# Kernel optimization log

Measured on AMD Instinct MI355X. Metric: run time of the kernel, lower is better.

Reference implementation:

```python
import jax, jax.numpy as jnp
import numpy as np

BATCH, N_MACS_PREV, CMS_PREV, NEUR_PREV = 256, 512, 8, 16
FILTER_LEN = 256
NUM_CMS, NUM_NEURONS = 32, 32
NUM_INPUTS = FILTER_LEN * CMS_PREV * NEUR_PREV  # 32768


def setup_inputs() -> dict:
    key = jax.random.key(0)
    k1, k2, k3 = jax.random.split(key, 3)
    x = jax.random.uniform(k1, (BATCH, N_MACS_PREV, CMS_PREV, NEUR_PREV), dtype=jnp.float32)
    input_filter = jax.random.randint(k2, (FILTER_LEN,), 0, N_MACS_PREV)
    # binary {0,1} weights, matching torch.randint(0, 2, ..., dtype=float32)
    weights = jax.random.randint(k3, (NUM_CMS, NUM_INPUTS, NUM_NEURONS), 0, 2).astype(jnp.float32)
    return {"x": x, "input_filter": input_filter, "weights": weights}


def reference(x, input_filter, weights):
    B = x.shape[0]
    # gather receptive field MACs and flatten: (B, num_inputs)
    xg = jnp.take(x, input_filter, axis=1).reshape(B, -1)
    # sum-normalize, nan_to_num handles all-zero rows (0/0 -> 0)
    xn = jnp.nan_to_num(xg / jnp.sum(xg, axis=-1, keepdims=True))
    # batched matmul: (B,I) x (C,I,N) -> (B,C,N)  (torch does (C,B,N) then permutes)
    acts = jnp.einsum('bi,cin->bcn', xn, weights)
    # familiarity-based softmax temperature
    familiarities = jnp.max(acts, axis=-1)          # (B, C)
    avg_fam = jnp.mean(familiarities)               # scalar
    softmax_temp = 1.0 / (avg_fam + 1e-4) - 1.0
    logits = acts / softmax_temp
    # categorical sample per (batch, cm); fixed key for determinism
    samples = jax.random.categorical(jax.random.key(42), logits, axis=-1)  # (B, C)
    # scatter one-hot write-out, int output as in torch
    out = jax.nn.one_hot(samples, NUM_NEURONS, dtype=jnp.int32)  # (B, C, N)
    return out
```

## Files before the change

### kernel.cpp

```cpp
#include <hip/hip_runtime.h>
#include <stdint.h>

#define BATCH 256
#define NMAC  512
#define ROWF  128
#define I_    32768
#define C_    32
#define N_    32
#define XROW  (NMAC * ROWF)
#define NCH   64

typedef float  f32x4  __attribute__((ext_vector_type(4)));
typedef __bf16 bf16x8 __attribute__((ext_vector_type(8)));

__device__ __forceinline__ uint32_t f2bf_rne(float f) {
    uint32_t u = __builtin_bit_cast(uint32_t, f);
    return (u + 0x7FFFu + ((u >> 16) & 1u)) >> 16;
}

__global__ __launch_bounds__(256) void k_sum(const float* __restrict__ x,
                                             const int* __restrict__ filt,
                                             float* __restrict__ S) {
    const int b = blockIdx.x;
    const int t = threadIdx.x;
    const float* xb = x + (size_t)b * XROW;
    float s = 0.f;
    for (int it = 0; it < 32; ++it) {
        int idx4 = it * 256 + t;
        int f = idx4 >> 5;
        int j4 = idx4 & 31;
        float4 v = *(const float4*)(xb + (size_t)filt[f] * ROWF + j4 * 4);
        s += v.x + v.y + v.z + v.w;
    }
    for (int o = 32; o > 0; o >>= 1) s += __shfl_down(s, o, 64);
    __shared__ float red[4];
    if ((t & 63) == 0) red[t >> 6] = s;
    __syncthreads();
    if (t == 0) S[b] = red[0] + red[1] + red[2] + red[3];
}

__global__ __launch_bounds__(256, 2) void k_gemm5(const float* __restrict__ x,
                                                  const int* __restrict__ filt,
                                                  const float* __restrict__ w,
                                                  float* __restrict__ part) {
    __shared__ __align__(16) unsigned short afr[32 * 512];
    __shared__ __align__(16) unsigned short wfr[8 * 512];
    __shared__ uint32_t wbits[4 * 512];

    const int t  = threadIdx.x;
    const int l  = t & 63;
    const int wv = t >> 6;
    const int chunk = blockIdx.x & 63;
    const int c0 = (blockIdx.x >> 6) * 4;

    f32x4 acc[4][8];
#pragma unroll
    for (int bt = 0; bt < 4; ++bt)
#pragma unroll
        for (int ct = 0; ct < 8; ++ct) acc[bt][ct] = f32x4{0.f, 0.f, 0.f, 0.f};

#pragma unroll
    for (int j = 0; j < 8; ++j) {
        int r  = j * 256 + t;
        int c  = r & 3;
        int io = r >> 2;
        const float4* wp = (const float4*)(w +
            ((size_t)(c0 + c) * I_ + chunk * 512 + io) * N_);
        uint32_t m = 0;
#pragma unroll
        for (int q = 0; q < 8; ++q) {
            float4 v = wp[q];
            m |= (v.x != 0.f ? 1u : 0u) << (q * 4 + 0);
            m |= (v.y != 0.f ? 1u : 0u) << (q * 4 + 1);
            m |= (v.z != 0.f ? 1u : 0u) << (q * 4 + 2);
            m |= (v.w != 0.f ? 1u : 0u) << (q * 4 + 3);
        }
        wbits[c * 512 + io] = m;
    }
    __syncthreads();

    const int ar     = t >> 3;
    const int ai     = t & 7;
    const int a_quad = ai >> 1;
    const int a_j    = (ai & 1) * 4;
    const int wn = t & 31;
    const int wc = t >> 5;

    for (int st = 0; st < 16; ++st) {
        const int ifull = chunk * 512 + st * 32;
        const int fidx  = filt[ifull >> 7];
        const int ioff  = ifull & 127;
        const float* xs = x + (size_t)fidx * ROWF + ioff;

#pragma unroll
        for (int q = 0; q < 8; ++q) {
            int sl = wc + 8 * q;
            int c  = sl >> 4;
            int il = (sl & 15) * 2;
            uint2 mm = *(const uint2*)&wbits[c * 512 + st * 32 + il];
            uint32_t pk = (((mm.x >> wn) & 1u) ? 0x00003F80u : 0u)
                        | (((mm.y >> wn) & 1u) ? 0x3F800000u : 0u);
            int lane = (il >> 3) * 16 + (wn & 15);
            int ct   = c * 2 + (wn >> 4);
            *(uint32_t*)&wfr[ct * 512 + lane * 8 + (il & 7)] = pk;
        }

#pragma unroll
        for (int rr = 0; rr < 8; ++rr) {
            int row = rr * 32 + ar;
            float4 v = *(const float4*)(xs + (size_t)row * XROW + ai * 4);
            uint32_t u0 = __builtin_bit_cast(uint32_t, v.x);
            uint32_t u1 = __builtin_bit_cast(uint32_t, v.y);
            uint32_t u2 = __builtin_bit_cast(uint32_t, v.z);
            uint32_t u3 = __builtin_bit_cast(uint32_t, v.w);
            float l0 = v.x - __builtin_bit_cast(float, u0 & 0xFFFF0000u);
            float l1 = v.y - __builtin_bit_cast(float, u1 & 0xFFFF0000u);
            float l2 = v.z - __builtin_bit_cast(float, u2 & 0xFFFF0000u);
            float l3 = v.w - __builtin_bit_cast(float, u3 & 0xFFFF0000u);
            uint2 hp, lp;
            hp.x = (u0 >> 16) | (u1 & 0xFFFF0000u);
            hp.y = (u2 >> 16) | (u3 & 0xFFFF0000u);
            lp.x = f2bf_rne(l0) | (f2bf_rne(l1) << 16);
            lp.y = f2bf_rne(l2) | (f2bf_rne(l3) << 16);
            int rt   = row >> 4;
            int lane = a_quad * 16 + (row & 15);
            int base = (rt * 2) * 512 + lane * 8 + a_j;
            *(uint2*)&afr[base]       = hp;
            *(uint2*)&afr[base + 512] = lp;
        }
        __syncthreads();

        bf16x8 av[4][2];
#pragma unroll
        for (int bt = 0; bt < 4; ++bt)
#pragma unroll
            for (int p = 0; p < 2; ++p)
                av[bt][p] = *(const bf16x8*)&afr[((wv * 4 + bt) * 2 + p) * 512 + l * 8];
        bf16x8 bv[8];
#pragma unroll
        for (int ct = 0; ct < 8; ++ct)
            bv[ct] = *(const bf16x8*)&wfr[ct * 512 + l * 8];
#pragma unroll
        for (int bt = 0; bt < 4; ++bt)
#pragma unroll
            for (int ct = 0; ct < 8; ++ct) {
                acc[bt][ct] = __builtin_amdgcn_mfma_f32_16x16x32_bf16(av[bt][0], bv[ct], acc[bt][ct], 0, 0, 0);
                acc[bt][ct] = __builtin_amdgcn_mfma_f32_16x16x32_bf16(av[bt][1], bv[ct], acc[bt][ct], 0, 0, 0);
            }
        __syncthreads();
    }

    const int quad = l >> 4, n15 = l & 15;
    float* dst = part + (size_t)chunk * (BATCH * C_ * N_);
#pragma unroll
    for (int bt = 0; bt < 4; ++bt) {
#pragma unroll
        for (int ct = 0; ct < 8; ++ct) {
            int c = c0 + (ct >> 1);
            int n = (ct & 1) * 16 + n15;
#pragma unroll
            for (int r = 0; r < 4; ++r) {
                int b = (wv * 4 + bt) * 16 + quad * 4 + r;
                dst[((size_t)b * C_ + c) * N_ + n] = acc[bt][ct][r];
            }
        }
    }
}

__global__ __launch_bounds__(256, 2) void k_gemm_fb(const float* __restrict__ x,
                                                    const int* __restrict__ filt,
                                                    const float* __restrict__ w,
                                                    float* __restrict__ raw) {
    __shared__ __align__(16) unsigned short afr[32 * 512];
    __shared__ __align__(16) unsigned short wfr[8 * 512];

    const int t  = threadIdx.x;
    const int l  = t & 63;
    const int wv = t >> 6;
    const int chunk = blockIdx.x & 63;
    const int c0 = (blockIdx.x >> 6) * 4;

    f32x4 acc[4][8];
#pragma unroll
    for (int bt = 0; bt < 4; ++bt)
#pragma unroll
        for (int ct = 0; ct < 8; ++ct) acc[bt][ct] = f32x4{0.f, 0.f, 0.f, 0.f};

    const int ar     = t >> 3;
    const int ai     = t & 7;
    const int a_quad = ai >> 1;
    const int a_j    = (ai & 1) * 4;
    const int wn = t & 31;
    const int wc = t >> 5;

    for (int st = 0; st < 16; ++st) {
        const int ifull = chunk * 512 + st * 32;
        const int fidx  = filt[ifull >> 7];
        const int ioff  = ifull & 127;
        const float* xs = x + (size_t)fidx * ROWF + ioff;

#pragma unroll
        for (int rr = 0; rr < 8; ++rr) {
            int row = rr * 32 + ar;
            float4 v = *(const float4*)(xs + (size_t)row * XROW + ai * 4);
            uint32_t u0 = __builtin_bit_cast(uint32_t, v.x);
            uint32_t u1 = __builtin_bit_cast(uint32_t, v.y);
            uint32_t u2 = __builtin_bit_cast(uint32_t, v.z);
            uint32_t u3 = __builtin_bit_cast(uint32_t, v.w);
            float l0 = v.x - __builtin_bit_cast(float, u0 & 0xFFFF0000u);
            float l1 = v.y - __builtin_bit_cast(float, u1 & 0xFFFF0000u);
            float l2 = v.z - __builtin_bit_cast(float, u2 & 0xFFFF0000u);
            float l3 = v.w - __builtin_bit_cast(float, u3 & 0xFFFF0000u);
            uint2 hp, lp;
            hp.x = (u0 >> 16) | (u1 & 0xFFFF0000u);
            hp.y = (u2 >> 16) | (u3 & 0xFFFF0000u);
            lp.x = f2bf_rne(l0) | (f2bf_rne(l1) << 16);
            lp.y = f2bf_rne(l2) | (f2bf_rne(l3) << 16);
            int rt   = row >> 4;
            int lane = a_quad * 16 + (row & 15);
            int base = (rt * 2) * 512 + lane * 8 + a_j;
            *(uint2*)&afr[base]       = hp;
            *(uint2*)&afr[base + 512] = lp;
        }
#pragma unroll
        for (int q = 0; q < 8; ++q) {
            int sl  = wc + 8 * q;
            int c   = sl >> 4;
            int il  = (sl & 15) * 2;
            const float* wp = w + ((size_t)(c0 + c) * I_ + ifull + il) * N_ + wn;
            uint32_t u0 = __builtin_bit_cast(uint32_t, wp[0]);
            uint32_t u1 = __builtin_bit_cast(uint32_t, wp[N_]);
            uint32_t pk = (u0 >> 16) | (u1 & 0xFFFF0000u);
            int lane = (il >> 3) * 16 + (wn & 15);
            int ct   = c * 2 + (wn >> 4);
            *(uint32_t*)&wfr[ct * 512 + lane * 8 + (il & 7)] = pk;
        }
        __syncthreads();

        bf16x8 av[4][2];
#pragma unroll
        for (int bt = 0; bt < 4; ++bt)
#pragma unroll
            for (int p = 0; p < 2; ++p)
                av[bt][p] = *(const bf16x8*)&afr[((wv * 4 + bt) * 2 + p) * 512 + l * 8];
        bf16x8 bv[8];
#pragma unroll
        for (int ct = 0; ct < 8; ++ct)
            bv[ct] = *(const bf16x8*)&wfr[ct * 512 + l * 8];
#pragma unroll
        for (int bt = 0; bt < 4; ++bt)
#pragma unroll
            for (int ct = 0; ct < 8; ++ct) {
                acc[bt][ct] = __builtin_amdgcn_mfma_f32_16x16x32_bf16(av[bt][0], bv[ct], acc[bt][ct], 0, 0, 0);
                acc[bt][ct] = __builtin_amdgcn_mfma_f32_16x16x32_bf16(av[bt][1], bv[ct], acc[bt][ct], 0, 0, 0);
            }
        __syncthreads();
    }

    const int quad = l >> 4, n15 = l & 15;
#pragma unroll
    for (int bt = 0; bt < 4; ++bt)
#pragma unroll
        for (int ct = 0; ct < 8; ++ct) {
            int c = c0 + (ct >> 1);
            int n = (ct & 1) * 16 + n15;
#pragma unroll
            for (int r = 0; r < 4; ++r) {
                int b = (wv * 4 + bt) * 16 + quad * 4 + r;
                atomicAdd(&raw[((size_t)b * C_ + c) * N_ + n], acc[bt][ct][r]);
            }
        }
}

__global__ __launch_bounds__(256) void k_reduce(const float* __restrict__ part,
                                                const float* __restrict__ S,
                                                float* __restrict__ raw,
                                                float* __restrict__ fam) {
    const int i4 = blockIdx.x * 256 + threadIdx.x;
    const f32x4* p = (const f32x4*)part;
    f32x4 s = f32x4{0.f, 0.f, 0.f, 0.f};
#pragma unroll 8
    for (int ch = 0; ch < NCH; ++ch) s += p[(size_t)ch * 65536 + i4];
    ((f32x4*)raw)[i4] = s;
    float m = fmaxf(fmaxf(s[0], s[1]), fmaxf(s[2], s[3]));
    m = fmaxf(m, __shfl_xor(m, 1, 64));
    m = fmaxf(m, __shfl_xor(m, 2, 64));
    m = fmaxf(m, __shfl_xor(m, 4, 64));
    int r = i4 >> 3;
    float v = ((i4 & 7) == 0) ? (m / S[r >> 5]) : 0.f;
    for (int o = 32; o > 0; o >>= 1) v += __shfl_down(v, o, 64);
    __shared__ float red[4];
    if ((threadIdx.x & 63) == 0) red[threadIdx.x >> 6] = v;
    __syncthreads();
    if (threadIdx.x == 0) atomicAdd(fam, red[0] + red[1] + red[2] + red[3]);
}

__global__ __launch_bounds__(256) void k_fam(const float* __restrict__ raw,
                                             const float* __restrict__ S,
                                             float* __restrict__ fam) {
    int r = blockIdx.x * 256 + threadIdx.x;
    const float4* ap = (const float4*)(raw + (size_t)r * N_);
    float m = -3.0e38f;
#pragma unroll
    for (int q = 0; q < 8; ++q) {
        float4 v = ap[q];
        m = fmaxf(m, fmaxf(fmaxf(v.x, v.y), fmaxf(v.z, v.w)));
    }
    m = m / S[r >> 5];
    for (int o = 32; o > 0; o >>= 1) m += __shfl_down(m, o, 64);
    __shared__ float red[4];
    if ((threadIdx.x & 63) == 0) red[threadIdx.x >> 6] = m;
    __syncthreads();
    if (threadIdx.x == 0) atomicAdd(fam, red[0] + red[1] + red[2] + red[3]);
}

__device__ __forceinline__ uint32_t rotl32(uint32_t x, uint32_t r) {
    return (x << r) | (x >> (32u - r));
}
__device__ __forceinline__ void threefry(uint32_t k0, uint32_t k1,
                                         uint32_t x0, uint32_t x1,
                                         uint32_t& o0, uint32_t& o1) {
    uint32_t ks2 = k0 ^ k1 ^ 0x1BD11BDAu;
    x0 += k0; x1 += k1;
    x0 += x1; x1 = rotl32(x1, 13); x1 ^= x0;
    x0 += x1; x1 = rotl32(x1, 15); x1 ^= x0;
    x0 += x1; x1 = rotl32(x1, 26); x1 ^= x0;
    x0 += x1; x1 = rotl32(x1, 6);  x1 ^= x0;
    x0 += k1; x1 += ks2 + 1u;
    x0 += x1; x1 = rotl32(x1, 17); x1 ^= x0;
    x0 += x1; x1 = rotl32(x1, 29); x1 ^= x0;
    x0 += x1; x1 = rotl32(x1, 16); x1 ^= x0;
    x0 += x1; x1 = rotl32(x1, 24); x1 ^= x0;
    x0 += ks2; x1 += k0 + 2u;
    x0 += x1; x1 = rotl32(x1, 13); x1 ^= x0;
    x0 += x1; x1 = rotl32(x1, 15); x1 ^= x0;
    x0 += x1; x1 = rotl32(x1, 26); x1 ^= x0;
    x0 += x1; x1 = rotl32(x1, 6);  x1 ^= x0;
    x0 += k0; x1 += k1 + 3u;
    x0 += x1; x1 = rotl32(x1, 17); x1 ^= x0;
    x0 += x1; x1 = rotl32(x1, 29); x1 ^= x0;
    x0 += x1; x1 = rotl32(x1, 16); x1 ^= x0;
    x0 += x1; x1 = rotl32(x1, 24); x1 ^= x0;
    x0 += k1; x1 += ks2 + 4u;
    x0 += x1; x1 = rotl32(x1, 13); x1 ^= x0;
    x0 += x1; x1 = rotl32(x1, 15); x1 ^= x0;
    x0 += x1; x1 = rotl32(x1, 26); x1 ^= x0;
    x0 += x1; x1 = rotl32(x1, 6);  x1 ^= x0;
    x0 += ks2; x1 += k0 + 5u;
    o0 = x0; o1 = x1;
}

__device__ __forceinline__ float gumbel_of(uint32_t bits) {
    uint32_t fb = (bits >> 9) | 0x3F800000u;
    float f = __builtin_bit_cast(float, fb) - 1.0f;
    float u = f + 1.17549435e-38f;
    return -logf(-logf(u));
}

__global__ __launch_bounds__(256) void k_sample(const float* __restrict__ raw,
                                                const float* __restrict__ S,
                                                const float* __restrict__ fam,
                                                int* __restrict__ out) {
    int r0 = blockIdx.x * 256 + threadIdx.x;
    int r1 = r0 + 4096;
    float avg  = fam[0] * (1.0f / 8192.0f);
    float temp = 1.0f / (avg + 1e-4f) - 1.0f;
    float sA = S[r0 >> 5], sB = S[r1 >> 5];
    const float* apA = raw + (size_t)r0 * N_;
    const float* apB = raw + (size_t)r1 * N_;

    float bestA = -3.4e38f, bestB = -3.4e38f;
    int biA = 0, biB = 0;
    for (int n = 0; n < 32; ++n) {
        uint32_t iA = (uint32_t)(r0 * 32 + n);
        uint32_t iB = (uint32_t)(r1 * 32 + n);
        uint32_t a0, a1, b0, b1;
        threefry(0u, 42u, 0u, iA, a0, a1);
        threefry(0u, 42u, 0u, iB, b0, b1);
        float vA = (apA[n] / sA) / temp + gumbel_of(a0 ^ a1);
        float vB = (apB[n] / sB) / temp + gumbel_of(b0 ^ b1);
        if (vA > bestA) { bestA = vA; biA = n; }
        if (vB > bestB) { bestB = vB; biB = n; }
    }
    int4* opA = (int4*)(out + (size_t)r0 * N_);
    int4* opB = (int4*)(out + (size_t)r1 * N_);
#pragma unroll
    for (int q = 0; q < 8; ++q) {
        int4 a, b;
        a.x = (q * 4 + 0) == biA; a.y = (q * 4 + 1) == biA;
        a.z = (q * 4 + 2) == biA; a.w = (q * 4 + 3) == biA;
        b.x = (q * 4 + 0) == biB; b.y = (q * 4 + 1) == biB;
        b.z = (q * 4 + 2) == biB; b.w = (q * 4 + 3) == biB;
        opA[q] = a; opB[q] = b;
    }
}

extern "C" void kernel_launch(void* const* d_in, const int* in_sizes, int n_in,
                              void* d_out, int out_size, void* d_ws, size_t ws_size,
                              hipStream_t stream) {
    const float* x    = (const float*)d_in[0];
    const int*   filt = (const int*)d_in[1];
    const float* w    = (const float*)d_in[2];
    int* out = (int*)d_out;

    char* ws = (char*)d_ws;
    float* raw  = (float*)ws;
    float* fam  = (float*)(ws + (1 << 20));
    float* S    = (float*)(ws + (1 << 20) + 128);
    float* part = (float*)(ws + (2u << 20));

    const size_t need_part = (2u << 20) + (size_t)NCH * (BATCH * C_ * N_) * sizeof(float);

    if (ws_size >= need_part) {
        hipMemsetAsync(ws + (1 << 20), 0, 128, stream);
        hipLaunchKernelGGL(k_sum,    dim3(256), dim3(256), 0, stream, x, filt, S);
        hipLaunchKernelGGL(k_gemm5,  dim3(512), dim3(256), 0, stream, x, filt, w, part);
        hipLaunchKernelGGL(k_reduce, dim3(256), dim3(256), 0, stream, part, S, raw, fam);
        hipLaunchKernelGGL(k_sample, dim3(16),  dim3(256), 0, stream, raw, S, fam, out);
    } else {
        hipMemsetAsync(ws, 0, (1 << 20) + 128, stream);
        hipLaunchKernelGGL(k_sum,    dim3(256), dim3(256), 0, stream, x, filt, S);
        hipLaunchKernelGGL(k_gemm_fb, dim3(512), dim3(256), 0, stream, x, filt, w, raw);
        hipLaunchKernelGGL(k_fam,    dim3(32),  dim3(256), 0, stream, raw, S, fam);
        hipLaunchKernelGGL(k_sample, dim3(16),  dim3(256), 0, stream, raw, S, fam, out);
    }
}
```

Baseline: 308.1 us.

## Fuse row-sum into GEMM launch and load weights per stage as bf16

```diff
diff --git a/kernel.cpp b/kernel.cpp
--- a/kernel.cpp
+++ b/kernel.cpp
@@ -18,66 +18,48 @@
     return (u + 0x7FFFu + ((u >> 16) & 1u)) >> 16;
 }
 
-__global__ __launch_bounds__(256) void k_sum(const float* __restrict__ x,
-                                             const int* __restrict__ filt,
-                                             float* __restrict__ S) {
-    const int b = blockIdx.x;
-    const int t = threadIdx.x;
-    const float* xb = x + (size_t)b * XROW;
-    float s = 0.f;
-    for (int it = 0; it < 32; ++it) {
-        int idx4 = it * 256 + t;
-        int f = idx4 >> 5;
-        int j4 = idx4 & 31;
-        float4 v = *(const float4*)(xb + (size_t)filt[f] * ROWF + j4 * 4);
-        s += v.x + v.y + v.z + v.w;
-    }
-    for (int o = 32; o > 0; o >>= 1) s += __shfl_down(s, o, 64);
-    __shared__ float red[4];
-    if ((t & 63) == 0) red[t >> 6] = s;
-    __syncthreads();
-    if (t == 0) S[b] = red[0] + red[1] + red[2] + red[3];
-}
-
-__global__ __launch_bounds__(256, 2) void k_gemm5(const float* __restrict__ x,
+__global__ __launch_bounds__(256, 2) void k_fused(const float* __restrict__ x,
                                                   const int* __restrict__ filt,
                                                   const float* __restrict__ w,
+                                                  float* __restrict__ S,
+                                                  float* __restrict__ fam,
                                                   float* __restrict__ part) {
     __shared__ __align__(16) unsigned short afr[32 * 512];
     __shared__ __align__(16) unsigned short wfr[8 * 512];
-    __shared__ uint32_t wbits[4 * 512];
-
-    const int t  = threadIdx.x;
+    __shared__ float red[4];
+
+    const int t = threadIdx.x;
+
+    if (blockIdx.x < 256) {
+        const int b = blockIdx.x;
+        if (b == 0 && t == 0) fam[0] = 0.f;
+        const float* xb = x + (size_t)b * XROW;
+        float s = 0.f;
+        for (int it = 0; it < 32; ++it) {
+            int idx4 = it * 256 + t;
+            int f = idx4 >> 5;
+            int j4 = idx4 & 31;
+            float4 v = *(const float4*)(xb + (size_t)filt[f] * ROWF + j4 * 4);
+            s += v.x + v.y + v.z + v.w;
+        }
+        for (int o = 32; o > 0; o >>= 1) s += __shfl_down(s, o, 64);
+        if ((t & 63) == 0) red[t >> 6] = s;
+        __syncthreads();
+        if (t == 0) S[b] = red[0] + red[1] + red[2] + red[3];
+        return;
+    }
+
+    const int bid = blockIdx.x - 256;
     const int l  = t & 63;
     const int wv = t >> 6;
-    const int chunk = blockIdx.x & 63;
-    const int c0 = (blockIdx.x >> 6) * 4;
+    const int chunk = bid & 63;
+    const int c0 = (bid >> 6) * 4;
 
     f32x4 acc[4][8];
 #pragma unroll
     for (int bt = 0; bt < 4; ++bt)
 #pragma unroll
         for (int ct = 0; ct < 8; ++ct) acc[bt][ct] = f32x4{0.f, 0.f, 0.f, 0.f};
-
-#pragma unroll
-    for (int j = 0; j < 8; ++j) {
-        int r  = j * 256 + t;
-        int c  = r & 3;
-        int io = r >> 2;
-        const float4* wp = (const float4*)(w +
-            ((size_t)(c0 + c) * I_ + chunk * 512 + io) * N_);
-        uint32_t m = 0;
-#pragma unroll
-        for (int q = 0; q < 8; ++q) {
-            float4 v = wp[q];
-            m |= (v.x != 0.f ? 1u : 0u) << (q * 4 + 0);
-            m |= (v.y != 0.f ? 1u : 0u) << (q * 4 + 1);
-            m |= (v.z != 0.f ? 1u : 0u) << (q * 4 + 2);
-            m |= (v.w != 0.f ? 1u : 0u) << (q * 4 + 3);
-        }
-        wbits[c * 512 + io] = m;
-    }
-    __syncthreads();
 
     const int ar     = t >> 3;
     const int ai     = t & 7;
@@ -91,19 +73,6 @@
         const int fidx  = filt[ifull >> 7];
         const int ioff  = ifull & 127;
         const float* xs = x + (size_t)fidx * ROWF + ioff;
-
-#pragma unroll
-        for (int q = 0; q < 8; ++q) {
-            int sl = wc + 8 * q;
-            int c  = sl >> 4;
-            int il = (sl & 15) * 2;
-            uint2 mm = *(const uint2*)&wbits[c * 512 + st * 32 + il];
-            uint32_t pk = (((mm.x >> wn) & 1u) ? 0x00003F80u : 0u)
-                        | (((mm.y >> wn) & 1u) ? 0x3F800000u : 0u);
-            int lane = (il >> 3) * 16 + (wn & 15);
-            int ct   = c * 2 + (wn >> 4);
-            *(uint32_t*)&wfr[ct * 512 + lane * 8 + (il & 7)] = pk;
-        }
 
 #pragma unroll
         for (int rr = 0; rr < 8; ++rr) {
@@ -128,6 +97,20 @@
             *(uint2*)&afr[base]       = hp;
             *(uint2*)&afr[base + 512] = lp;
         }
+
+#pragma unroll
+        for (int q = 0; q < 8; ++q) {
+            int sl  = wc + 8 * q;
+            int c   = sl >> 4;
+            int il  = (sl & 15) * 2;
+            const float* wp = w + ((size_t)(c0 + c) * I_ + ifull + il) * N_ + wn;
+            uint32_t u0 = __builtin_bit_cast(uint32_t, wp[0]);
+            uint32_t u1 = __builtin_bit_cast(uint32_t, wp[N_]);
+            uint32_t pk = (u0 >> 16) | (u1 & 0xFFFF0000u);
+            int lane = (il >> 3) * 16 + (wn & 15);
+            int ct   = c * 2 + (wn >> 4);
+            *(uint32_t*)&wfr[ct * 512 + lane * 8 + (il & 7)] = pk;
+        }
         __syncthreads();
 
         bf16x8 av[4][2];
@@ -165,6 +148,29 @@
             }
         }
     }
+}
+
+__global__ __launch_bounds__(256) void k_sum(const float* __restrict__ x,
+                                             const int* __restrict__ filt,
+                                             float* __restrict__ S,
+                                             float* __restrict__ fam) {
+    const int b = blockIdx.x;
+    const int t = threadIdx.x;
+    if (b == 0 && t == 0) fam[0] = 0.f;
+    const float* xb = x + (size_t)b * XROW;
+    float s = 0.f;
+    for (int it = 0; it < 32; ++it) {
+        int idx4 = it * 256 + t;
+        int f = idx4 >> 5;
+        int j4 = idx4 & 31;
+        float4 v = *(const float4*)(xb + (size_t)filt[f] * ROWF + j4 * 4);
+        s += v.x + v.y + v.z + v.w;
+    }
+    for (int o = 32; o > 0; o >>= 1) s += __shfl_down(s, o, 64);
+    __shared__ float red[4];
+    if ((t & 63) == 0) red[t >> 6] = s;
+    __syncthreads();
+    if (t == 0) S[b] = red[0] + red[1] + red[2] + red[3];
 }
 
 __global__ __launch_bounds__(256, 2) void k_gemm_fb(const float* __restrict__ x,
@@ -409,17 +415,16 @@
     float* S    = (float*)(ws + (1 << 20) + 128);
     float* part = (float*)(ws + (2u << 20));
 
-    const size_t need_part = (2u << 20) + (size_t)NCH * (BATCH * C_ * N_) * sizeof(float);
-
-    if (ws_size >= need_part) {
-        hipMemsetAsync(ws + (1 << 20), 0, 128, stream);
-        hipLaunchKernelGGL(k_sum,    dim3(256), dim3(256), 0, stream, x, filt, S);
-        hipLaunchKernelGGL(k_gemm5,  dim3(512), dim3(256), 0, stream, x, filt, w, part);
+    const size_t need = (2u << 20) + (size_t)NCH * (BATCH * C_ * N_) * sizeof(float);
+    const int use_part = (ws_size >= need) ? 1 : 0;
+
+    if (use_part) {
+        hipLaunchKernelGGL(k_fused,  dim3(768), dim3(256), 0, stream, x, filt, w, S, fam, part);
         hipLaunchKernelGGL(k_reduce, dim3(256), dim3(256), 0, stream, part, S, raw, fam);
         hipLaunchKernelGGL(k_sample, dim3(16),  dim3(256), 0, stream, raw, S, fam, out);
     } else {
         hipMemsetAsync(ws, 0, (1 << 20) + 128, stream);
-        hipLaunchKernelGGL(k_sum,    dim3(256), dim3(256), 0, stream, x, filt, S);
+        hipLaunchKernelGGL(k_sum,    dim3(256), dim3(256), 0, stream, x, filt, S, fam);
         hipLaunchKernelGGL(k_gemm_fb, dim3(512), dim3(256), 0, stream, x, filt, w, raw);
         hipLaunchKernelGGL(k_fam,    dim3(32),  dim3(256), 0, stream, raw, S, fam);
         hipLaunchKernelGGL(k_sample, dim3(16),  dim3(256), 0, stream, raw, S, fam, out);
```

New measurement: 278.2 us (median of 2 runs). -9.7%, faster.
